# Kernel optimization log

Hardware: AMD Instinct MI355X
Metric: run time of the kernel (lower is better)

## Reference

```python
import jax, jax.numpy as jnp
import numpy as np

# Hyperparameters mirroring init_kwargs
MAX_ITERS = 100      # ADMM outer iterations
RHO = 1.0            # ADMM penalty
INNER = 20           # PGD steps per x-subproblem
STEP = 5e-05         # fixed PGD step (x_inner_step given, so no svdvals branch)


def setup_inputs() -> dict:
    key = jax.random.key(0)
    kA, kb, kc = jax.random.split(key, 3)
    m, n = 2048, 4096
    A = jax.random.normal(kA, (m, n), dtype=jnp.float32)
    b = jax.random.uniform(kb, (m,), dtype=jnp.float32)
    c = jax.random.uniform(kc, (n,), dtype=jnp.float32)
    return {"A": A, "b": b, "c": c}


def _admm(A, b, c):
    m, n = A.shape

    def outer(carry, _):
        x, s, u = carry
        r = s + b - u  # target for the x-subproblem residual

        # PGD on: min_{x>=0} c^T x + (rho/2)||A x - r||^2
        def pgd(x, _):
            g = c + RHO * (A.T @ (A @ x - r))
            return jnp.maximum(x - STEP * g, 0.0), None

        x, _ = jax.lax.scan(pgd, x, None, length=INNER)

        Ax = A @ x
        s = jnp.maximum(Ax - b + u, 0.0)   # slack update (projection onto >=0)
        u = u + (Ax - s - b)               # scaled dual update
        return (x, s, u), None

    init = (jnp.zeros((n,), A.dtype), jnp.zeros((m,), A.dtype), jnp.zeros((m,), A.dtype))
    (x, s, u), _ = jax.lax.scan(outer, init, None, length=MAX_ITERS)
    lambda_kkt = -RHO * u
    return x, s, u, lambda_kkt


def reference(A, b, c):
    # return_history=False -> torch module returns (x, s, u, lambda_kkt, None);
    # we return the 4 tensor outputs.
    return _admm(A, b, c)
```

## Files before the change

### kernel.cpp

```cpp
#include <hip/hip_runtime.h>
#include <hip/hip_cooperative_groups.h>

namespace cg = cooperative_groups;

#define M_ROWS 2048
#define N_COLS 4096
#define RHO_C 1.0f
#define STEP_C 5e-05f
#define MAX_ITERS_C 100
#define INNER_C 20

__device__ __forceinline__ float aload(const float* p) {
    return __hip_atomic_load(p, __ATOMIC_RELAXED, __HIP_MEMORY_SCOPE_AGENT);
}
__device__ __forceinline__ void astore(float* p, float v) {
    __hip_atomic_store(p, v, __ATOMIC_RELAXED, __HIP_MEMORY_SCOPE_AGENT);
}
__device__ __forceinline__ float2 aload2(const float* p) {
    unsigned long long v = __hip_atomic_load(
        (const unsigned long long*)p, __ATOMIC_RELAXED,
        __HIP_MEMORY_SCOPE_AGENT);
    union { unsigned long long u; float2 f; } c; c.u = v; return c.f;
}

__device__ inline void fast_barrier(unsigned* bs, int blk, unsigned n) {
    __syncthreads();
    if (threadIdx.x == 0) {
        __builtin_amdgcn_fence(__ATOMIC_RELEASE, "workgroup");
        unsigned* leaf = bs + ((blk & 7) << 5);
        unsigned* root = bs + 256;
        unsigned* ep   = bs + 288;
        unsigned old = __hip_atomic_fetch_add(leaf, 1u, __ATOMIC_RELAXED,
                                              __HIP_MEMORY_SCOPE_AGENT);
        if (old == n * 32u + 31u) {
            unsigned ro = __hip_atomic_fetch_add(root, 1u, __ATOMIC_RELAXED,
                                                 __HIP_MEMORY_SCOPE_AGENT);
            if (ro == n * 8u + 7u)
                __hip_atomic_fetch_add(ep, 1u, __ATOMIC_RELAXED,
                                       __HIP_MEMORY_SCOPE_AGENT);
        }
        while (__hip_atomic_load(ep, __ATOMIC_RELAXED,
                                 __HIP_MEMORY_SCOPE_AGENT) <= n)
            __builtin_amdgcn_s_sleep(1);
        __builtin_amdgcn_fence(__ATOMIC_ACQUIRE, "workgroup");
    }
    __syncthreads();
}

__global__ __launch_bounds__(1024) void admm_gram(
    const float* __restrict__ A, const float* __restrict__ bvec,
    const float* __restrict__ cvec, float* __restrict__ out,
    float* __restrict__ x0, float* __restrict__ x1,
    float* __restrict__ rt, unsigned* __restrict__ bstate)
{
    cg::grid_group grid = cg::this_grid();
    const int tid  = threadIdx.x;
    const int blk  = blockIdx.x;
    const int lane = tid & 63;
    const int wave = tid >> 6;
    const int cgp  = wave >> 2;
    const int rq   = wave & 3;

    __shared__ float  abuf[4 * N_COLS];
    __shared__ float4 xs4[1024];
    __shared__ float  red[4][16];
    __shared__ float4 gred[64];
    __shared__ float  wl[16], cw[16];
    __shared__ float  sv[8], uv[8], tpart[16];

    float* xs = reinterpret_cast<float*>(xs4);
    const float4* A4 = reinterpret_cast<const float4*>(A);
    float4* abuf4 = reinterpret_cast<float4*>(abuf);

    if (tid < 16) {
        cw[tid] = cvec[blk * 16 + tid];
        astore(&x0[blk * 16 + tid], 0.0f);
    }
    if (tid < 8) {
        sv[tid] = 0.0f; uv[tid] = 0.0f;
        astore(&rt[blk * 8 + tid], bvec[blk * 8 + tid]);
    }
    if (blk == 0 && tid < 320) bstate[tid] = 0u;

    float accM[4][16];
    #pragma unroll
    for (int r = 0; r < 4; ++r)
        #pragma unroll
        for (int k = 0; k < 16; ++k) accM[r][k] = 0.0f;

    for (int i0 = 0; i0 < M_ROWS; i0 += 4) {
        #pragma unroll
        for (int ii = 0; ii < 4; ++ii)
            abuf4[ii * 1024 + tid] = A4[(size_t)(i0 + ii) * 1024 + tid];
        __syncthreads();
        #pragma unroll
        for (int ii = 0; ii < 4; ++ii) {
            const float*  row  = abuf + ii * N_COLS;
            const float4* row4 = abuf4 + ii * 1024;
            float4 av[4];
            #pragma unroll
            for (int q = 0; q < 4; ++q)
                av[q] = row4[256 * cgp + 64 * q + lane];
            float cb[4];
            #pragma unroll
            for (int r = 0; r < 4; ++r) cb[r] = row[blk * 16 + rq * 4 + r];
            #pragma unroll
            for (int r = 0; r < 4; ++r)
                #pragma unroll
                for (int q = 0; q < 4; ++q) {
                    accM[r][4 * q + 0] = fmaf(cb[r], av[q].x, accM[r][4 * q + 0]);
                    accM[r][4 * q + 1] = fmaf(cb[r], av[q].y, accM[r][4 * q + 1]);
                    accM[r][4 * q + 2] = fmaf(cb[r], av[q].z, accM[r][4 * q + 2]);
                    accM[r][4 * q + 3] = fmaf(cb[r], av[q].w, accM[r][4 * q + 3]);
                }
        }
        __syncthreads();
    }

    grid.sync();
    unsigned bar_n = 0;

    for (int outer = 0; outer < MAX_ITERS_C; ++outer) {
        abuf[tid]        = aload(&rt[tid]);
        abuf[tid + 1024] = aload(&rt[tid + 1024]);
        __syncthreads();
        {
            const int p = tid >> 2, gq = tid & 3;
            float4 acc = {0.f, 0.f, 0.f, 0.f};
            #pragma unroll
            for (int k2 = 0; k2 < 8; ++k2) {
                const int i = p + 256 * k2;
                const float tv = abuf[i];
                float4 a = A4[(size_t)i * 1024 + blk * 4 + gq];
                acc.x = fmaf(a.x, tv, acc.x); acc.y = fmaf(a.y, tv, acc.y);
                acc.z = fmaf(a.z, tv, acc.z); acc.w = fmaf(a.w, tv, acc.w);
            }
            #pragma unroll
            for (int off = 4; off < 64; off <<= 1) {
                acc.x += __shfl_xor(acc.x, off);
                acc.y += __shfl_xor(acc.y, off);
                acc.z += __shfl_xor(acc.z, off);
                acc.w += __shfl_xor(acc.w, off);
            }
            if ((lane >> 2) == 0) gred[wave * 4 + gq] = acc;
        }
        __syncthreads();
        if (tid < 4) {
            float4 tot = {0.f, 0.f, 0.f, 0.f};
            #pragma unroll
            for (int w = 0; w < 16; ++w) {
                float4 v = gred[w * 4 + tid];
                tot.x += v.x; tot.y += v.y; tot.z += v.z; tot.w += v.w;
            }
            wl[tid * 4 + 0] = tot.x; wl[tid * 4 + 1] = tot.y;
            wl[tid * 4 + 2] = tot.z; wl[tid * 4 + 3] = tot.w;
        }
        __syncthreads();

        for (int inner = 0; inner < INNER_C; ++inner) {
            const float* xsrc = (inner & 1) ? x1 : x0;
            float*       xdst = (inner & 1) ? x0 : x1;

            {
                float2 lo = aload2(xsrc + 4 * tid);
                float2 hi = aload2(xsrc + 4 * tid + 2);
                xs4[tid] = make_float4(lo.x, lo.y, hi.x, hi.y);
            }
            __syncthreads();

            float4 xq[4];
            #pragma unroll
            for (int q = 0; q < 4; ++q)
                xq[q] = xs4[256 * cgp + 64 * q + lane];

            float4 pd = {0.f, 0.f, 0.f, 0.f};
            #pragma unroll
            for (int q = 0; q < 4; ++q) {
                pd.x = fmaf(accM[0][4*q+0], xq[q].x, pd.x);
                pd.x = fmaf(accM[0][4*q+1], xq[q].y, pd.x);
                pd.x = fmaf(accM[0][4*q+2], xq[q].z, pd.x);
                pd.x = fmaf(accM[0][4*q+3], xq[q].w, pd.x);
                pd.y = fmaf(accM[1][4*q+0], xq[q].x, pd.y);
                pd.y = fmaf(accM[1][4*q+1], xq[q].y, pd.y);
                pd.y = fmaf(accM[1][4*q+2], xq[q].z, pd.y);
                pd.y = fmaf(accM[1][4*q+3], xq[q].w, pd.y);
                pd.z = fmaf(accM[2][4*q+0], xq[q].x, pd.z);
                pd.z = fmaf(accM[2][4*q+1], xq[q].y, pd.z);
                pd.z = fmaf(accM[2][4*q+2], xq[q].z, pd.z);
                pd.z = fmaf(accM[2][4*q+3], xq[q].w, pd.z);
                pd.w = fmaf(accM[3][4*q+0], xq[q].x, pd.w);
                pd.w = fmaf(accM[3][4*q+1], xq[q].y, pd.w);
                pd.w = fmaf(accM[3][4*q+2], xq[q].z, pd.w);
                pd.w = fmaf(accM[3][4*q+3], xq[q].w, pd.w);
            }

            #pragma unroll
            for (int off = 32; off; off >>= 1) {
                pd.x += __shfl_xor(pd.x, off);
                pd.y += __shfl_xor(pd.y, off);
                pd.z += __shfl_xor(pd.z, off);
                pd.w += __shfl_xor(pd.w, off);
            }
            if (lane == 0) {
                red[cgp][rq * 4 + 0] = pd.x;
                red[cgp][rq * 4 + 1] = pd.y;
                red[cgp][rq * 4 + 2] = pd.z;
                red[cgp][rq * 4 + 3] = pd.w;
            }
            __syncthreads();

            if (tid < 16) {
                const float y = red[0][tid] + red[1][tid]
                              + red[2][tid] + red[3][tid];
                const float g = cw[tid] + RHO_C * (y - wl[tid]);
                float xn = xs[blk * 16 + tid] - STEP_C * g;
                xn = xn > 0.f ? xn : 0.f;
                astore(&xdst[blk * 16 + tid], xn);
            }
            fast_barrier(bstate, blk, bar_n); ++bar_n;
        }

        {
            float2 lo = aload2(x0 + 4 * tid);
            float2 hi = aload2(x0 + 4 * tid + 2);
            xs4[tid] = make_float4(lo.x, lo.y, hi.x, hi.y);
        }
        __syncthreads();
        {
            const int r = blk * 8 + (wave >> 1), h = wave & 1;
            const float4* Ar = A4 + (size_t)r * 1024 + h * 512;
            const float4* xh = xs4 + h * 512;
            float4 acc = {0.f, 0.f, 0.f, 0.f};
            #pragma unroll
            for (int it = 0; it < 8; ++it) {
                float4 a = Ar[it * 64 + lane], xv = xh[it * 64 + lane];
                acc.x = fmaf(a.x, xv.x, acc.x); acc.y = fmaf(a.y, xv.y, acc.y);
                acc.z = fmaf(a.z, xv.z, acc.z); acc.w = fmaf(a.w, xv.w, acc.w);
            }
            float d = acc.x + acc.y + acc.z + acc.w;
            #pragma unroll
            for (int off = 32; off; off >>= 1) d += __shfl_xor(d, off);
            if (lane == 0) tpart[wave] = d;
        }
        __syncthreads();
        if (tid < 8) {
            const int i = blk * 8 + tid;
            const float a  = tpart[2 * tid] + tpart[2 * tid + 1];
            const float bb = bvec[i];
            const float uu = uv[tid];
            float sn = a - bb + uu; sn = sn > 0.f ? sn : 0.f;
            const float un = uu + a - sn - bb;
            sv[tid] = sn; uv[tid] = un;
            astore(&rt[i], sn + bb - un);
        }
        fast_barrier(bstate, blk, bar_n); ++bar_n;
    }

    if (tid < 16) out[blk * 16 + tid] = aload(&x0[blk * 16 + tid]);
    if (tid < 8) {
        const int i = blk * 8 + tid;
        out[4096 + i] = sv[tid];
        out[6144 + i] = uv[tid];
        out[8192 + i] = -uv[tid];
    }
}

extern "C" void kernel_launch(void* const* d_in, const int* in_sizes, int n_in,
                              void* d_out, int out_size, void* d_ws, size_t ws_size,
                              hipStream_t stream) {
    const float* A    = (const float*)d_in[0];
    const float* bvec = (const float*)d_in[1];
    const float* cvec = (const float*)d_in[2];
    float* out = (float*)d_out;

    float* ws = (float*)d_ws;
    float* x0 = ws;
    float* x1 = ws + 4096;
    float* rt = ws + 8192;
    unsigned* bstate = (unsigned*)(ws + 12288);

    void* args[] = { (void*)&A, (void*)&bvec, (void*)&cvec, (void*)&out,
                     (void*)&x0, (void*)&x1, (void*)&rt, (void*)&bstate };
    hipError_t err = hipLaunchCooperativeKernel((const void*)admm_gram,
                               dim3(256), dim3(1024), args, 0, stream);
    (void)err;
}
```

Measured before the change: 10.82 ms.

## Replace grid barriers with tagged dataflow slots and add packed A-slice for A^T r

Removes the hierarchical atomic grid barrier between PGD steps and between outer iterations. Each x and r value is now published into a double-buffered 64-bit slot carrying an iteration tag, and consumers spin only until the values they need carry the expected tag. This cuts the barrier round-trip latency and lets blocks move ahead independently, at the cost of more polling traffic on 64-bit slots. Separately, when the workspace is large enough, each block keeps a packed copy of its 16-column slice of A during the Gram build, so the per-outer-iteration A^T r reads contiguous data instead of strided rows of A. Correctness depends on the tag protocol across the double buffers and on stale tags left in the workspace from earlier launches.

```diff
diff --git a/kernel.cpp b/kernel.cpp
--- a/kernel.cpp
+++ b/kernel.cpp
@@ -1,7 +1,6 @@
 #include <hip/hip_runtime.h>
-#include <hip/hip_cooperative_groups.h>
-
-namespace cg = cooperative_groups;
+
+typedef unsigned long long u64;
 
 #define M_ROWS 2048
 #define N_COLS 4096
@@ -10,50 +9,44 @@
 #define MAX_ITERS_C 100
 #define INNER_C 20
 
-__device__ __forceinline__ float aload(const float* p) {
+__device__ __forceinline__ void slot_push(u64* p, float v, unsigned tag) {
+    u64 val = ((u64)tag << 32) | (u64)__float_as_uint(v);
+    __hip_atomic_store(p, val, __ATOMIC_RELAXED, __HIP_MEMORY_SCOPE_AGENT);
+}
+__device__ __forceinline__ u64 slot_ld(const u64* p) {
     return __hip_atomic_load(p, __ATOMIC_RELAXED, __HIP_MEMORY_SCOPE_AGENT);
 }
-__device__ __forceinline__ void astore(float* p, float v) {
-    __hip_atomic_store(p, v, __ATOMIC_RELAXED, __HIP_MEMORY_SCOPE_AGENT);
-}
-__device__ __forceinline__ float2 aload2(const float* p) {
-    unsigned long long v = __hip_atomic_load(
-        (const unsigned long long*)p, __ATOMIC_RELAXED,
-        __HIP_MEMORY_SCOPE_AGENT);
-    union { unsigned long long u; float2 f; } c; c.u = v; return c.f;
-}
-
-__device__ inline void fast_barrier(unsigned* bs, int blk, unsigned n) {
-    __syncthreads();
-    if (threadIdx.x == 0) {
-        __builtin_amdgcn_fence(__ATOMIC_RELEASE, "workgroup");
-        unsigned* leaf = bs + ((blk & 7) << 5);
-        unsigned* root = bs + 256;
-        unsigned* ep   = bs + 288;
-        unsigned old = __hip_atomic_fetch_add(leaf, 1u, __ATOMIC_RELAXED,
-                                              __HIP_MEMORY_SCOPE_AGENT);
-        if (old == n * 32u + 31u) {
-            unsigned ro = __hip_atomic_fetch_add(root, 1u, __ATOMIC_RELAXED,
-                                                 __HIP_MEMORY_SCOPE_AGENT);
-            if (ro == n * 8u + 7u)
-                __hip_atomic_fetch_add(ep, 1u, __ATOMIC_RELAXED,
-                                       __HIP_MEMORY_SCOPE_AGENT);
-        }
-        while (__hip_atomic_load(ep, __ATOMIC_RELAXED,
-                                 __HIP_MEMORY_SCOPE_AGENT) <= n)
-            __builtin_amdgcn_s_sleep(1);
-        __builtin_amdgcn_fence(__ATOMIC_ACQUIRE, "workgroup");
-    }
-    __syncthreads();
-}
-
-__global__ __launch_bounds__(1024) void admm_gram(
+__device__ __forceinline__ float4 slot_poll4(const u64* p, unsigned tag) {
+    u64 a, b, c, d;
+    for (;;) {
+        a = slot_ld(p); b = slot_ld(p + 1);
+        c = slot_ld(p + 2); d = slot_ld(p + 3);
+        if (((unsigned)(a >> 32) == tag) & ((unsigned)(b >> 32) == tag) &
+            ((unsigned)(c >> 32) == tag) & ((unsigned)(d >> 32) == tag))
+            break;
+        __builtin_amdgcn_s_sleep(1);
+    }
+    return make_float4(__uint_as_float((unsigned)a), __uint_as_float((unsigned)b),
+                       __uint_as_float((unsigned)c), __uint_as_float((unsigned)d));
+}
+__device__ __forceinline__ float2 slot_poll2(const u64* p, unsigned tag) {
+    u64 a, b;
+    for (;;) {
+        a = slot_ld(p); b = slot_ld(p + 1);
+        if (((unsigned)(a >> 32) == tag) & ((unsigned)(b >> 32) == tag)) break;
+        __builtin_amdgcn_s_sleep(1);
+    }
+    return make_float2(__uint_as_float((unsigned)a), __uint_as_float((unsigned)b));
+}
+
+__global__ __launch_bounds__(1024) void admm_df(
     const float* __restrict__ A, const float* __restrict__ bvec,
     const float* __restrict__ cvec, float* __restrict__ out,
-    float* __restrict__ x0, float* __restrict__ x1,
-    float* __restrict__ rt, unsigned* __restrict__ bstate)
+    u64* __restrict__ xslot,
+    u64* __restrict__ rslot,
+    float* __restrict__ atp,
+    int use_packed)
 {
-    cg::grid_group grid = cg::this_grid();
     const int tid  = threadIdx.x;
     const int blk  = blockIdx.x;
     const int lane = tid & 63;
@@ -71,16 +64,16 @@
     float* xs = reinterpret_cast<float*>(xs4);
     const float4* A4 = reinterpret_cast<const float4*>(A);
     float4* abuf4 = reinterpret_cast<float4*>(abuf);
+    float* atpB = atp + (size_t)blk * 32768;
 
     if (tid < 16) {
         cw[tid] = cvec[blk * 16 + tid];
-        astore(&x0[blk * 16 + tid], 0.0f);
+        slot_push(&xslot[blk * 16 + tid], 0.0f, 0u);
     }
     if (tid < 8) {
         sv[tid] = 0.0f; uv[tid] = 0.0f;
-        astore(&rt[blk * 8 + tid], bvec[blk * 8 + tid]);
-    }
-    if (blk == 0 && tid < 320) bstate[tid] = 0u;
+        slot_push(&rslot[blk * 8 + tid], bvec[blk * 8 + tid], 0u);
+    }
 
     float accM[4][16];
     #pragma unroll
@@ -93,6 +86,10 @@
         for (int ii = 0; ii < 4; ++ii)
             abuf4[ii * 1024 + tid] = A4[(size_t)(i0 + ii) * 1024 + tid];
         __syncthreads();
+        if (use_packed && tid < 64) {
+            const int ii = tid >> 4, j = tid & 15;
+            atpB[(i0 + ii) * 16 + j] = abuf[ii * N_COLS + blk * 16 + j];
+        }
         #pragma unroll
         for (int ii = 0; ii < 4; ++ii) {
             const float*  row  = abuf + ii * N_COLS;
@@ -108,23 +105,46 @@
             for (int r = 0; r < 4; ++r)
                 #pragma unroll
                 for (int q = 0; q < 4; ++q) {
-                    accM[r][4 * q + 0] = fmaf(cb[r], av[q].x, accM[r][4 * q + 0]);
-                    accM[r][4 * q + 1] = fmaf(cb[r], av[q].y, accM[r][4 * q + 1]);
-                    accM[r][4 * q + 2] = fmaf(cb[r], av[q].z, accM[r][4 * q + 2]);
-                    accM[r][4 * q + 3] = fmaf(cb[r], av[q].w, accM[r][4 * q + 3]);
+                    accM[r][4*q+0] = fmaf(cb[r], av[q].x, accM[r][4*q+0]);
+                    accM[r][4*q+1] = fmaf(cb[r], av[q].y, accM[r][4*q+1]);
+                    accM[r][4*q+2] = fmaf(cb[r], av[q].z, accM[r][4*q+2]);
+                    accM[r][4*q+3] = fmaf(cb[r], av[q].w, accM[r][4*q+3]);
                 }
         }
         __syncthreads();
     }
 
-    grid.sync();
-    unsigned bar_n = 0;
-
     for (int outer = 0; outer < MAX_ITERS_C; ++outer) {
-        abuf[tid]        = aload(&rt[tid]);
-        abuf[tid + 1024] = aload(&rt[tid + 1024]);
-        __syncthreads();
         {
+            const u64* rb = rslot + (outer & 1) * M_ROWS;
+            float2 rv = slot_poll2(&rb[2 * tid], (unsigned)outer);
+            abuf[2 * tid]     = rv.x;
+            abuf[2 * tid + 1] = rv.y;
+        }
+        __syncthreads();
+
+        if (use_packed) {
+            const int rr = tid >> 4, j = tid & 15;
+            float p = 0.f;
+            #pragma unroll 4
+            for (int k = 0; k < 32; ++k) {
+                const int i = rr + (k << 6);
+                p = fmaf(atpB[(i << 4) + j], abuf[i], p);
+            }
+            float* wred = abuf + 2048;
+            wred[tid] = p;
+            __syncthreads();
+            if (tid < 256)
+                wred[tid] = wred[tid] + wred[tid + 256]
+                          + wred[tid + 512] + wred[tid + 768];
+            __syncthreads();
+            if (tid < 16) {
+                float s = 0.f;
+                #pragma unroll
+                for (int r2 = 0; r2 < 16; ++r2) s += wred[r2 * 16 + tid];
+                wl[tid] = s;
+            }
+        } else {
             const int p = tid >> 2, gq = tid & 3;
             float4 acc = {0.f, 0.f, 0.f, 0.f};
             #pragma unroll
@@ -143,29 +163,28 @@
                 acc.w += __shfl_xor(acc.w, off);
             }
             if ((lane >> 2) == 0) gred[wave * 4 + gq] = acc;
-        }
-        __syncthreads();
-        if (tid < 4) {
-            float4 tot = {0.f, 0.f, 0.f, 0.f};
-            #pragma unroll
-            for (int w = 0; w < 16; ++w) {
-                float4 v = gred[w * 4 + tid];
-                tot.x += v.x; tot.y += v.y; tot.z += v.z; tot.w += v.w;
-            }
-            wl[tid * 4 + 0] = tot.x; wl[tid * 4 + 1] = tot.y;
-            wl[tid * 4 + 2] = tot.z; wl[tid * 4 + 3] = tot.w;
+            __syncthreads();
+            if (tid < 4) {
+                float4 tot = {0.f, 0.f, 0.f, 0.f};
+                #pragma unroll
+                for (int w = 0; w < 16; ++w) {
+                    float4 v = gred[w * 4 + tid];
+                    tot.x += v.x; tot.y += v.y; tot.z += v.z; tot.w += v.w;
+                }
+                wl[tid * 4 + 0] = tot.x; wl[tid * 4 + 1] = tot.y;
+                wl[tid * 4 + 2] = tot.z; wl[tid * 4 + 3] = tot.w;
+            }
         }
         __syncthreads();
 
         for (int inner = 0; inner < INNER_C; ++inner) {
-            const float* xsrc = (inner & 1) ? x1 : x0;
-            float*       xdst = (inner & 1) ? x0 : x1;
-
-            {
-                float2 lo = aload2(xsrc + 4 * tid);
-                float2 hi = aload2(xsrc + 4 * tid + 2);
-                xs4[tid] = make_float4(lo.x, lo.y, hi.x, hi.y);
-            }
+            const unsigned gs = (unsigned)(outer * INNER_C + inner);
+            const u64* xrb = xslot + (gs & 1) * N_COLS;
+            u64*       xwb = xslot + ((gs + 1) & 1) * N_COLS;
+
+            float4 xv = slot_poll4(&xrb[4 * tid], gs);
+            __syncthreads();
+            xs4[tid] = xv;
             __syncthreads();
 
             float4 xq[4];
@@ -193,7 +212,6 @@
                 pd.w = fmaf(accM[3][4*q+2], xq[q].z, pd.w);
                 pd.w = fmaf(accM[3][4*q+3], xq[q].w, pd.w);
             }
-
             #pragma unroll
             for (int off = 32; off; off >>= 1) {
                 pd.x += __shfl_xor(pd.x, off);
@@ -208,24 +226,24 @@
                 red[cgp][rq * 4 + 3] = pd.w;
             }
             __syncthreads();
-
             if (tid < 16) {
                 const float y = red[0][tid] + red[1][tid]
                               + red[2][tid] + red[3][tid];
                 const float g = cw[tid] + RHO_C * (y - wl[tid]);
                 float xn = xs[blk * 16 + tid] - STEP_C * g;
                 xn = xn > 0.f ? xn : 0.f;
-                astore(&xdst[blk * 16 + tid], xn);
-            }
-            fast_barrier(bstate, blk, bar_n); ++bar_n;
+                slot_push(&xwb[blk * 16 + tid], xn, gs + 1);
+            }
         }
 
         {
-            float2 lo = aload2(x0 + 4 * tid);
-            float2 hi = aload2(x0 + 4 * tid + 2);
-            xs4[tid] = make_float4(lo.x, lo.y, hi.x, hi.y);
-        }
-        __syncthreads();
+            const unsigned tagAx = (unsigned)((outer + 1) * INNER_C);
+            const u64* xrb = xslot + (tagAx & 1) * N_COLS;
+            float4 xv = slot_poll4(&xrb[4 * tid], tagAx);
+            __syncthreads();
+            xs4[tid] = xv;
+            __syncthreads();
+        }
         {
             const int r = blk * 8 + (wave >> 1), h = wave & 1;
             const float4* Ar = A4 + (size_t)r * 1024 + h * 512;
@@ -251,12 +269,13 @@
             float sn = a - bb + uu; sn = sn > 0.f ? sn : 0.f;
             const float un = uu + a - sn - bb;
             sv[tid] = sn; uv[tid] = un;
-            astore(&rt[i], sn + bb - un);
-        }
-        fast_barrier(bstate, blk, bar_n); ++bar_n;
-    }
-
-    if (tid < 16) out[blk * 16 + tid] = aload(&x0[blk * 16 + tid]);
+            slot_push(&rslot[((outer + 1) & 1) * M_ROWS + i],
+                      sn + bb - un, (unsigned)(outer + 1));
+        }
+        __syncthreads();
+    }
+
+    if (tid < 16) out[blk * 16 + tid] = xs[blk * 16 + tid];
     if (tid < 8) {
         const int i = blk * 8 + tid;
         out[4096 + i] = sv[tid];
@@ -273,15 +292,16 @@
     const float* cvec = (const float*)d_in[2];
     float* out = (float*)d_out;
 
-    float* ws = (float*)d_ws;
-    float* x0 = ws;
-    float* x1 = ws + 4096;
-    float* rt = ws + 8192;
-    unsigned* bstate = (unsigned*)(ws + 12288);
+    char* ws = (char*)d_ws;
+    u64*   xslot = (u64*)(ws);
+    u64*   rslot = (u64*)(ws + 65536);
+    float* atp   = (float*)(ws + 131072);
+    int use_packed = (ws_size >= (size_t)131072 + (size_t)256 * 32768 * 4) ? 1 : 0;
 
     void* args[] = { (void*)&A, (void*)&bvec, (void*)&cvec, (void*)&out,
-                     (void*)&x0, (void*)&x1, (void*)&rt, (void*)&bstate };
-    hipError_t err = hipLaunchCooperativeKernel((const void*)admm_gram,
+                     (void*)&xslot, (void*)&rslot, (void*)&atp,
+                     (void*)&use_packed };
+    hipError_t err = hipLaunchCooperativeKernel((const void*)admm_df,
                                dim3(256), dim3(1024), args, 0, stream);
     (void)err;
 }
```

Result: slower. 12.42 ms (+14.8%).

## Replace tree grid barrier with per-block epoch tags and polling

Applied to the files above, without the earlier changes.

Replaces the hierarchical atomic-counter grid barrier with per-block monotonic tags: each block publishes its slice of x or r into a double buffer and then bumps its tag. Consumers wait with one wave polling all 256 tags through a ballot-min before reading. This drops the serialized leaf/root/epoch atomic chain and lets a block continue as soon as every producer has posted. In exchange each block now issues many tag loads per step, and the double-buffer reuse relies on the tag protocol for correctness (release ordering between data and tag is only relaxed plus __syncthreads).

```diff
diff --git a/kernel.cpp b/kernel.cpp
--- a/kernel.cpp
+++ b/kernel.cpp
@@ -2,6 +2,7 @@
 #include <hip/hip_cooperative_groups.h>
 
 namespace cg = cooperative_groups;
+typedef unsigned int u32;
 
 #define M_ROWS 2048
 #define N_COLS 4096
@@ -22,36 +23,33 @@
         __HIP_MEMORY_SCOPE_AGENT);
     union { unsigned long long u; float2 f; } c; c.u = v; return c.f;
 }
-
-__device__ inline void fast_barrier(unsigned* bs, int blk, unsigned n) {
-    __syncthreads();
-    if (threadIdx.x == 0) {
-        __builtin_amdgcn_fence(__ATOMIC_RELEASE, "workgroup");
-        unsigned* leaf = bs + ((blk & 7) << 5);
-        unsigned* root = bs + 256;
-        unsigned* ep   = bs + 288;
-        unsigned old = __hip_atomic_fetch_add(leaf, 1u, __ATOMIC_RELAXED,
-                                              __HIP_MEMORY_SCOPE_AGENT);
-        if (old == n * 32u + 31u) {
-            unsigned ro = __hip_atomic_fetch_add(root, 1u, __ATOMIC_RELAXED,
-                                                 __HIP_MEMORY_SCOPE_AGENT);
-            if (ro == n * 8u + 7u)
-                __hip_atomic_fetch_add(ep, 1u, __ATOMIC_RELAXED,
-                                       __HIP_MEMORY_SCOPE_AGENT);
-        }
-        while (__hip_atomic_load(ep, __ATOMIC_RELAXED,
-                                 __HIP_MEMORY_SCOPE_AGENT) <= n)
-            __builtin_amdgcn_s_sleep(1);
-        __builtin_amdgcn_fence(__ATOMIC_ACQUIRE, "workgroup");
-    }
-    __syncthreads();
-}
-
-__global__ __launch_bounds__(1024) void admm_gram(
+__device__ __forceinline__ u32 aloadu(const u32* p) {
+    return __hip_atomic_load(p, __ATOMIC_RELAXED, __HIP_MEMORY_SCOPE_AGENT);
+}
+__device__ __forceinline__ void astoreu(u32* p, u32 v) {
+    __hip_atomic_store(p, v, __ATOMIC_RELAXED, __HIP_MEMORY_SCOPE_AGENT);
+}
+
+__device__ __forceinline__ void poll256(const u32* tags, u32 need, int lane) {
+    const u32* p = tags + 4 * lane;
+    for (;;) {
+        u32 t0 = aloadu(p);     u32 t1 = aloadu(p + 1);
+        u32 t2 = aloadu(p + 2); u32 t3 = aloadu(p + 3);
+        u32 mn = t0 < t1 ? t0 : t1;
+        u32 mn2 = t2 < t3 ? t2 : t3;
+        mn = mn < mn2 ? mn : mn2;
+        if (__ballot(mn < need) == 0ull) return;
+        __builtin_amdgcn_s_sleep(1);
+    }
+}
+
+__global__ __launch_bounds__(1024) void admm_tag(
     const float* __restrict__ A, const float* __restrict__ bvec,
     const float* __restrict__ cvec, float* __restrict__ out,
-    float* __restrict__ x0, float* __restrict__ x1,
-    float* __restrict__ rt, unsigned* __restrict__ bstate)
+    float* __restrict__ xbuf,
+    float* __restrict__ rtb,
+    u32* __restrict__ xtag,
+    u32* __restrict__ rtag)
 {
     cg::grid_group grid = cg::this_grid();
     const int tid  = threadIdx.x;
@@ -72,15 +70,9 @@
     const float4* A4 = reinterpret_cast<const float4*>(A);
     float4* abuf4 = reinterpret_cast<float4*>(abuf);
 
-    if (tid < 16) {
-        cw[tid] = cvec[blk * 16 + tid];
-        astore(&x0[blk * 16 + tid], 0.0f);
-    }
-    if (tid < 8) {
-        sv[tid] = 0.0f; uv[tid] = 0.0f;
-        astore(&rt[blk * 8 + tid], bvec[blk * 8 + tid]);
-    }
-    if (blk == 0 && tid < 320) bstate[tid] = 0u;
+    if (tid < 16) cw[tid] = cvec[blk * 16 + tid];
+    if (tid < 8) { sv[tid] = 0.0f; uv[tid] = 0.0f; }
+    if (tid == 0) { astoreu(&xtag[blk], 0u); astoreu(&rtag[blk], 0u); }
 
     float accM[4][16];
     #pragma unroll
@@ -108,22 +100,31 @@
             for (int r = 0; r < 4; ++r)
                 #pragma unroll
                 for (int q = 0; q < 4; ++q) {
-                    accM[r][4 * q + 0] = fmaf(cb[r], av[q].x, accM[r][4 * q + 0]);
-                    accM[r][4 * q + 1] = fmaf(cb[r], av[q].y, accM[r][4 * q + 1]);
-                    accM[r][4 * q + 2] = fmaf(cb[r], av[q].z, accM[r][4 * q + 2]);
-                    accM[r][4 * q + 3] = fmaf(cb[r], av[q].w, accM[r][4 * q + 3]);
+                    accM[r][4*q+0] = fmaf(cb[r], av[q].x, accM[r][4*q+0]);
+                    accM[r][4*q+1] = fmaf(cb[r], av[q].y, accM[r][4*q+1]);
+                    accM[r][4*q+2] = fmaf(cb[r], av[q].z, accM[r][4*q+2]);
+                    accM[r][4*q+3] = fmaf(cb[r], av[q].w, accM[r][4*q+3]);
                 }
         }
         __syncthreads();
     }
 
     grid.sync();
-    unsigned bar_n = 0;
 
     for (int outer = 0; outer < MAX_ITERS_C; ++outer) {
-        abuf[tid]        = aload(&rt[tid]);
-        abuf[tid + 1024] = aload(&rt[tid + 1024]);
-        __syncthreads();
+        if (outer == 0) {
+            abuf[2 * tid]     = bvec[2 * tid];
+            abuf[2 * tid + 1] = bvec[2 * tid + 1];
+        } else {
+            if (wave == 0) poll256(rtag, (u32)outer, lane);
+            __syncthreads();
+            const float* rb = rtb + (outer & 1) * M_ROWS;
+            float2 rv = aload2(rb + 2 * tid);
+            abuf[2 * tid]     = rv.x;
+            abuf[2 * tid + 1] = rv.y;
+        }
+        __syncthreads();
+
         {
             const int p = tid >> 2, gq = tid & 3;
             float4 acc = {0.f, 0.f, 0.f, 0.f};
@@ -158,15 +159,20 @@
         __syncthreads();
 
         for (int inner = 0; inner < INNER_C; ++inner) {
-            const float* xsrc = (inner & 1) ? x1 : x0;
-            float*       xdst = (inner & 1) ? x0 : x1;
-
-            {
-                float2 lo = aload2(xsrc + 4 * tid);
-                float2 hi = aload2(xsrc + 4 * tid + 2);
+            const u32 gs = (u32)(outer * INNER_C + inner);
+
+            if (outer == 0 && inner == 0) {
+                xs4[tid] = make_float4(0.f, 0.f, 0.f, 0.f);
+                __syncthreads();
+            } else if (inner > 0) {
+                if (wave == 0) poll256(xtag, gs, lane);
+                __syncthreads();
+                const float* xb = xbuf + (gs & 1) * N_COLS;
+                float2 lo = aload2(xb + 4 * tid);
+                float2 hi = aload2(xb + 4 * tid + 2);
                 xs4[tid] = make_float4(lo.x, lo.y, hi.x, hi.y);
-            }
-            __syncthreads();
+                __syncthreads();
+            }
 
             float4 xq[4];
             #pragma unroll
@@ -193,7 +199,6 @@
                 pd.w = fmaf(accM[3][4*q+2], xq[q].z, pd.w);
                 pd.w = fmaf(accM[3][4*q+3], xq[q].w, pd.w);
             }
-
             #pragma unroll
             for (int off = 32; off; off >>= 1) {
                 pd.x += __shfl_xor(pd.x, off);
@@ -215,17 +220,22 @@
                 const float g = cw[tid] + RHO_C * (y - wl[tid]);
                 float xn = xs[blk * 16 + tid] - STEP_C * g;
                 xn = xn > 0.f ? xn : 0.f;
-                astore(&xdst[blk * 16 + tid], xn);
-            }
-            fast_barrier(bstate, blk, bar_n); ++bar_n;
+                astore(&xbuf[((gs + 1) & 1) * N_COLS + blk * 16 + tid], xn);
+            }
+            __syncthreads();
+            if (tid == 0) astoreu(&xtag[blk], gs + 1);
         }
 
         {
-            float2 lo = aload2(x0 + 4 * tid);
-            float2 hi = aload2(x0 + 4 * tid + 2);
+            const u32 gsf = (u32)((outer + 1) * INNER_C);
+            if (wave == 0) poll256(xtag, gsf, lane);
+            __syncthreads();
+            const float* xb = xbuf + (gsf & 1) * N_COLS;
+            float2 lo = aload2(xb + 4 * tid);
+            float2 hi = aload2(xb + 4 * tid + 2);
             xs4[tid] = make_float4(lo.x, lo.y, hi.x, hi.y);
-        }
-        __syncthreads();
+            __syncthreads();
+        }
         {
             const int r = blk * 8 + (wave >> 1), h = wave & 1;
             const float4* Ar = A4 + (size_t)r * 1024 + h * 512;
@@ -251,12 +261,13 @@
             float sn = a - bb + uu; sn = sn > 0.f ? sn : 0.f;
             const float un = uu + a - sn - bb;
             sv[tid] = sn; uv[tid] = un;
-            astore(&rt[i], sn + bb - un);
-        }
-        fast_barrier(bstate, blk, bar_n); ++bar_n;
-    }
-
-    if (tid < 16) out[blk * 16 + tid] = aload(&x0[blk * 16 + tid]);
+            astore(&rtb[((outer + 1) & 1) * M_ROWS + i], sn + bb - un);
+        }
+        __syncthreads();
+        if (tid == 0) astoreu(&rtag[blk], (u32)(outer + 1));
+    }
+
+    if (tid < 16) out[blk * 16 + tid] = xs[blk * 16 + tid];
     if (tid < 8) {
         const int i = blk * 8 + tid;
         out[4096 + i] = sv[tid];
@@ -273,15 +284,15 @@
     const float* cvec = (const float*)d_in[2];
     float* out = (float*)d_out;
 
-    float* ws = (float*)d_ws;
-    float* x0 = ws;
-    float* x1 = ws + 4096;
-    float* rt = ws + 8192;
-    unsigned* bstate = (unsigned*)(ws + 12288);
+    float* ws   = (float*)d_ws;
+    float* xbuf = ws;
+    float* rtb  = ws + 8192;
+    u32*   xtag = (u32*)(ws + 12288);
+    u32*   rtag = (u32*)(ws + 12288 + 256);
 
     void* args[] = { (void*)&A, (void*)&bvec, (void*)&cvec, (void*)&out,
-                     (void*)&x0, (void*)&x1, (void*)&rt, (void*)&bstate };
-    hipError_t err = hipLaunchCooperativeKernel((const void*)admm_gram,
+                     (void*)&xbuf, (void*)&rtb, (void*)&xtag, (void*)&rtag };
+    hipError_t err = hipLaunchCooperativeKernel((const void*)admm_tag,
                                dim3(256), dim3(1024), args, 0, stream);
     (void)err;
 }
```

New measurement: 11.94 ms. 10.3% more time.
